# Optimization experiments

Hardware: AMD Instinct MI355X
Metric: run time of the kernel (lower is better)

## Reference

```python
import jax, jax.numpy as jnp
import numpy as np

B, N, FIN, FOUT = 8, 2048, 128, 128


def setup_inputs() -> dict:
    key = jax.random.key(0)
    k1, k2, k3, k4, k5 = jax.random.split(key, 5)
    x = jax.random.normal(k1, (B, N, FIN), dtype=jnp.float32)
    adj = jax.random.randint(k2, (N, N), 0, 2, dtype=jnp.int32)
    # W stored [in, out] (transpose of torch Linear weight; same math via x @ W)
    W = jax.random.normal(k3, (FIN, FOUT), dtype=jnp.float32) * (1.0 / np.sqrt(FIN))
    # a: Linear(2*out, 1) split into src/dst halves: a([h_i,h_j]) = h_i@a_src + h_j@a_dst
    a_src = jax.random.normal(k4, (FOUT,), dtype=jnp.float32) * 0.1
    a_dst = jax.random.normal(k5, (FOUT,), dtype=jnp.float32) * 0.1
    return {"x": x, "adj": adj, "W": W, "a_src": a_src, "a_dst": a_dst}


def reference(x, adj, W, a_src, a_dst):
    # h: [B, N, FOUT]
    h = jnp.einsum('bnf,fo->bno', x, W)
    # attention logits e_ij = LeakyReLU(a_src.h_i + a_dst.h_j), built by broadcast
    s_i = jnp.einsum('bno,o->bn', h, a_src)  # [B, N]
    s_j = jnp.einsum('bno,o->bn', h, a_dst)  # [B, N]
    e = jax.nn.leaky_relu(s_i[:, :, None] + s_j[:, None, :], negative_slope=0.2)  # [B,N,N]
    scores = jnp.where(adj[None, :, :] == 0, -jnp.inf, e)
    attn = jax.nn.softmax(scores, axis=-1)
    attn = jnp.nan_to_num(attn, nan=0.0)  # rows with no neighbors -> all zeros
    # dropout is identity in eval mode
    out = jnp.einsum('bij,bjo->bio', attn, h)  # [B, N, FOUT]
    return out
```

## Files before the change

kernel.cpp:

```cpp
#include <hip/hip_runtime.h>
#include <math.h>

#define BATCH 8
#define NN 2048
#define FF 128

typedef __attribute__((ext_vector_type(4))) float f32x4;
typedef _Float16 half8 __attribute__((ext_vector_type(8)));

__device__ __forceinline__ unsigned short h2u(_Float16 h) {
    return __builtin_bit_cast(unsigned short, h);
}

__device__ __forceinline__ void h_split(float f, unsigned short& hi, unsigned short& lo) {
    const _Float16 hh = (_Float16)f;
    hi = h2u(hh);
    lo = h2u((_Float16)(f - (float)hh));
}

__global__ __launch_bounds__(256) void k_prep(const int* __restrict__ adj,
                                              const float* __restrict__ W,
                                              unsigned short* __restrict__ Wf_hi,
                                              unsigned short* __restrict__ Wf_lo,
                                              unsigned* __restrict__ amT) {
    const int t = threadIdx.x;
    const int bx = blockIdx.x;
    if (bx < 512) {
        const int w = t >> 6, lane = t & 63;
        const int row = bx * 4 + w;
        const int* __restrict__ ar = adj + (size_t)row * NN;
        #pragma unroll 8
        for (int seg = 0; seg < 32; ++seg) {
            const unsigned long long m = __ballot(ar[seg * 64 + lane] != 0);
            if (lane == 0)  amT[(size_t)(seg * 2) * NN + row] = (unsigned)m;
            if (lane == 32) amT[(size_t)(seg * 2 + 1) * NN + row] = (unsigned)(m >> 32);
        }
    } else {
        #pragma unroll
        for (int e = 0; e < 8; ++e) {
            const int fi = (bx - 512) * 2048 + e * 256 + t;
            const int j = fi & 7, ln = (fi >> 3) & 63, nt = (fi >> 9) & 7, ks = fi >> 12;
            const int k = ks * 32 + (ln >> 4) * 8 + j;
            const int col = nt * 16 + (ln & 15);
            unsigned short hh, hl;
            h_split(W[k * FF + col], hh, hl);
            Wf_hi[fi] = hh;
            Wf_lo[fi] = hl;
        }
    }
}

__global__ __launch_bounds__(256) void k_h(const float* __restrict__ x,
                                           const unsigned short* __restrict__ Wf_hi,
                                           const unsigned short* __restrict__ Wf_lo,
                                           const float* __restrict__ a_src,
                                           const float* __restrict__ a_dst,
                                           unsigned short* __restrict__ hF,
                                           float* __restrict__ Eg,  float* __restrict__ E2g,
                                           float* __restrict__ Sg,  float* __restrict__ S2g) {
    __shared__ float sred[4 * 16];
    __shared__ float dred[4 * 16];

    const int t = threadIdx.x;
    const int w = t >> 6, lane = t & 63;
    const int nl = lane & 15, quad = lane >> 4;
    const int row0 = blockIdx.x * 16;
    const int b = row0 >> 11, jloc0 = row0 & 2047;
    const int gr = row0 + nl;
    const int nt0 = w * 2;

    f32x4 acc[2] = {{0.f,0.f,0.f,0.f},{0.f,0.f,0.f,0.f}};

    #pragma unroll
    for (int ks = 0; ks < 4; ++ks) {
        const float4 xa = *reinterpret_cast<const float4*>(&x[(size_t)gr * FF + ks * 32 + quad * 8]);
        const float4 xb = *reinterpret_cast<const float4*>(&x[(size_t)gr * FF + ks * 32 + quad * 8 + 4]);
        const float xv[8] = {xa.x, xa.y, xa.z, xa.w, xb.x, xb.y, xb.z, xb.w};
        half8 ah, al;
        #pragma unroll
        for (int i = 0; i < 8; ++i) {
            const _Float16 hh = (_Float16)xv[i];
            ah[i] = hh;
            al[i] = (_Float16)(xv[i] - (float)hh);
        }
        #pragma unroll
        for (int nn = 0; nn < 2; ++nn) {
            const int bo = ((ks * 8 + nt0 + nn) * 64 + lane) * 8;
            const half8 bh = *reinterpret_cast<const half8*>(&Wf_hi[bo]);
            const half8 bl = *reinterpret_cast<const half8*>(&Wf_lo[bo]);
            acc[nn] = __builtin_amdgcn_mfma_f32_16x16x32_f16(ah, bh, acc[nn], 0, 0, 0);
            acc[nn] = __builtin_amdgcn_mfma_f32_16x16x32_f16(al, bh, acc[nn], 0, 0, 0);
            acc[nn] = __builtin_amdgcn_mfma_f32_16x16x32_f16(ah, bl, acc[nn], 0, 0, 0);
        }
    }

    const int jloc = jloc0 + quad * 4;
    const int jg = jloc >> 3, u0 = jloc & 7;
    #pragma unroll
    for (int nn = 0; nn < 2; ++nn) {
        ushort4 hv;
        hv.x = h2u((_Float16)acc[nn][0]);
        hv.y = h2u((_Float16)acc[nn][1]);
        hv.z = h2u((_Float16)acc[nn][2]);
        hv.w = h2u((_Float16)acc[nn][3]);
        *reinterpret_cast<ushort4*>(&hF[(size_t)b * 262144 + (nt0 + nn) * 32768 + jg * 128 + nl * 8 + u0]) = hv;
    }

    float as[2], ad[2];
    #pragma unroll
    for (int nn = 0; nn < 2; ++nn) {
        const int col = (nt0 + nn) * 16 + nl;
        as[nn] = a_src[col];
        ad[nn] = a_dst[col];
    }
    #pragma unroll
    for (int r = 0; r < 4; ++r) {
        float sp = acc[0][r] * as[0] + acc[1][r] * as[1];
        float dp = acc[0][r] * ad[0] + acc[1][r] * ad[1];
        #pragma unroll
        for (int off = 8; off >= 1; off >>= 1) {
            sp += __shfl_xor(sp, off, 16);
            dp += __shfl_xor(dp, off, 16);
        }
        if (nl == 0) {
            sred[w * 16 + quad * 4 + r] = sp;
            dred[w * 16 + quad * 4 + r] = dp;
        }
    }
    __syncthreads();
    if (t < 16) {
        const float sp = sred[t] + sred[16 + t] + sred[32 + t] + sred[48 + t];
        const float dp = dred[t] + dred[16 + t] + dred[32 + t] + dred[48 + t];
        const int row = row0 + t;
        Sg[row]  = __expf(sp - 2.f);
        S2g[row] = __expf(0.2f * sp - 2.f);
        Eg[row]  = __expf(dp - 2.f);
        E2g[row] = __expf(0.2f * dp - 2.f);
    }
}

__global__ __launch_bounds__(512, 4) void k_attn(const unsigned short* __restrict__ hF,
                                                 const unsigned* __restrict__ amT,
                                                 const float* __restrict__ Eg,
                                                 const float* __restrict__ E2g,
                                                 const float* __restrict__ Sg,
                                                 const float* __restrict__ S2g,
                                                 float* __restrict__ P,
                                                 float* __restrict__ L) {
    __shared__ float E_l[1024];
    __shared__ float E2_l[1024];
    __shared__ unsigned am_l[32 * 64];
    __shared__ unsigned short pA[2 * 64 * 72];

    const int t = threadIdx.x;
    const int b = blockIdx.y;
    const int i0 = blockIdx.x * 64;
    const int jh = blockIdx.z;
    const int jbase = jh * 1024;

    *reinterpret_cast<float2*>(&E_l[t * 2])  = *reinterpret_cast<const float2*>(&Eg[(size_t)b * NN + jbase + t * 2]);
    *reinterpret_cast<float2*>(&E2_l[t * 2]) = *reinterpret_cast<const float2*>(&E2g[(size_t)b * NN + jbase + t * 2]);
    #pragma unroll
    for (int k = 0; k < 4; ++k) {
        const int idx = k * 512 + t;
        am_l[idx] = amT[(size_t)(jh * 32 + (idx >> 6)) * NN + i0 + (idx & 63)];
    }
    __syncthreads();

    const int rp = t >> 4, jw4 = t & 15;
    const int ra = rp * 2, rb = ra + 1;
    const float Sa  = Sg[(size_t)b * NN + i0 + ra];
    const float S2a = S2g[(size_t)b * NN + i0 + ra];
    const float Sb  = Sg[(size_t)b * NN + i0 + rb];
    const float S2b = S2g[(size_t)b * NN + i0 + rb];
    const int bitb = (jw4 & 7) * 4;
    const int pwo = ra * 72 + jw4 * 4;

    const int w = t >> 6, lane = t & 63;
    const int nl = lane & 15, quad = lane >> 4;
    const int mtp = w & 1, ntp = w >> 1;
    const unsigned short* __restrict__ hFb = hF + (size_t)b * 262144;
    int bofs[2], aofs[2];
    #pragma unroll
    for (int nn = 0; nn < 2; ++nn) bofs[nn] = (ntp + nn * 4) * 32768 + (jbase + quad * 8) * 16 + nl * 8;
    #pragma unroll
    for (int mm = 0; mm < 2; ++mm) aofs[mm] = ((mtp + mm * 2) * 16 + nl) * 72 + quad * 8;

    f32x4 acc[2][2] = {{{0.f,0.f,0.f,0.f},{0.f,0.f,0.f,0.f}},{{0.f,0.f,0.f,0.f},{0.f,0.f,0.f,0.f}}};
    f32x4 lac[2] = {{0.f,0.f,0.f,0.f},{0.f,0.f,0.f,0.f}};
    half8 ones;
    #pragma unroll
    for (int i = 0; i < 8; ++i) ones[i] = (_Float16)1.f;

    for (int tt = 0; tt < 16; ++tt) {
        const int buf = tt & 1;
        const int jofs = tt * 1024;

        half8 bfr[2][2];
        #pragma unroll
        for (int nn = 0; nn < 2; ++nn) {
            bfr[nn][0] = *reinterpret_cast<const half8*>(hFb + bofs[nn] + jofs);
            bfr[nn][1] = *reinterpret_cast<const half8*>(hFb + bofs[nn] + jofs + 512);
        }

        {
            const int jb = tt * 64 + jw4 * 4;
            const float4 ej4  = *reinterpret_cast<const float4*>(&E_l[jb]);
            const float4 e2j4 = *reinterpret_cast<const float4*>(&E2_l[jb]);
            const uint2 mw = *reinterpret_cast<const uint2*>(&am_l[(tt * 2 + (jw4 >> 3)) * 64 + ra]);
            const float ejA[4]  = {ej4.x, ej4.y, ej4.z, ej4.w};
            const float e2jA[4] = {e2j4.x, e2j4.y, e2j4.z, e2j4.w};
            ushort4 ha, hb;
            #pragma unroll
            for (int jj = 0; jj < 4; ++jj) {
                const float ua = fmaxf(Sa * ejA[jj], S2a * e2jA[jj]);
                const float ub = fmaxf(Sb * ejA[jj], S2b * e2jA[jj]);
                const float pa = ((mw.x >> (bitb + jj)) & 1u) ? ua : 0.f;
                const float pb = ((mw.y >> (bitb + jj)) & 1u) ? ub : 0.f;
                ((unsigned short*)&ha)[jj] = h2u((_Float16)pa);
                ((unsigned short*)&hb)[jj] = h2u((_Float16)pb);
            }
            *reinterpret_cast<ushort4*>(&pA[buf * 4608 + pwo]) = ha;
            *reinterpret_cast<ushort4*>(&pA[buf * 4608 + pwo + 72]) = hb;
        }

        __syncthreads();

        half8 afr[2][2];
        #pragma unroll
        for (int mm = 0; mm < 2; ++mm) {
            afr[mm][0] = *reinterpret_cast<const half8*>(&pA[buf * 4608 + aofs[mm]]);
            afr[mm][1] = *reinterpret_cast<const half8*>(&pA[buf * 4608 + aofs[mm] + 32]);
        }
        #pragma unroll
        for (int mm = 0; mm < 2; ++mm) {
            #pragma unroll
            for (int kh = 0; kh < 2; ++kh) {
                lac[mm] = __builtin_amdgcn_mfma_f32_16x16x32_f16(afr[mm][kh], ones, lac[mm], 0, 0, 0);
                acc[mm][0] = __builtin_amdgcn_mfma_f32_16x16x32_f16(afr[mm][kh], bfr[0][kh], acc[mm][0], 0, 0, 0);
                acc[mm][1] = __builtin_amdgcn_mfma_f32_16x16x32_f16(afr[mm][kh], bfr[1][kh], acc[mm][1], 0, 0, 0);
            }
        }
    }

    float* __restrict__ Pb = P + ((size_t)jh * BATCH + b) * 262144;
    float* __restrict__ Lb = L + ((size_t)jh * BATCH + b) * 2048;
    #pragma unroll
    for (int mm = 0; mm < 2; ++mm) {
        const int lrow = (mtp + mm * 2) * 16 + quad * 4;
        #pragma unroll
        for (int r = 0; r < 4; ++r) {
            #pragma unroll
            for (int nn = 0; nn < 2; ++nn) {
                const int col = (ntp + nn * 4) * 16 + nl;
                Pb[(size_t)(i0 + lrow + r) * FF + col] = acc[mm][nn][r];
            }
            if (nl == 0 && ntp == 0) Lb[i0 + lrow + r] = lac[mm][r];
        }
    }
}

__global__ __launch_bounds__(256) void k_comb(const float* __restrict__ P,
                                              const float* __restrict__ L,
                                              float* __restrict__ out) {
    const int g0 = blockIdx.x * 512 + threadIdx.x;
    #pragma unroll
    for (int it = 0; it < 2; ++it) {
        const int g = g0 + it * 256;
        const size_t flat = (size_t)g * 4;
        const int row = (int)(flat >> 7);
        const float l = L[row] + L[16384 + row];
        const float inv = (l > 0.f) ? 1.f / l : 0.f;
        const float4 p0 = *reinterpret_cast<const float4*>(&P[flat]);
        const float4 p1 = *reinterpret_cast<const float4*>(&P[2097152 + flat]);
        *reinterpret_cast<float4*>(&out[flat]) =
            make_float4((p0.x + p1.x) * inv, (p0.y + p1.y) * inv,
                        (p0.z + p1.z) * inv, (p0.w + p1.w) * inv);
    }
}

extern "C" void kernel_launch(void* const* d_in, const int* in_sizes, int n_in,
                              void* d_out, int out_size, void* d_ws, size_t ws_size,
                              hipStream_t stream) {
    const float* x     = (const float*)d_in[0];
    const int*   adj   = (const int*)d_in[1];
    const float* W     = (const float*)d_in[2];
    const float* a_src = (const float*)d_in[3];
    const float* a_dst = (const float*)d_in[4];
    float* out = (float*)d_out;

    unsigned short* hF    = (unsigned short*)d_ws;
    unsigned short* Wf_hi = hF + 2097152;
    unsigned short* Wf_lo = Wf_hi + 16384;
    float* Eg  = (float*)(Wf_lo + 16384);
    float* E2g = Eg + 16384;
    float* Sg  = E2g + 16384;
    float* S2g = Sg + 16384;
    unsigned* amT = (unsigned*)(S2g + 16384);
    float* P = (float*)(amT + 131072);
    float* L = P + 4194304;

    k_prep<<<520, 256, 0, stream>>>(adj, W, Wf_hi, Wf_lo, amT);
    k_h<<<1024, 256, 0, stream>>>(x, Wf_hi, Wf_lo, a_src, a_dst, hF, Eg, E2g, Sg, S2g);
    k_attn<<<dim3(32, BATCH, 2), 512, 0, stream>>>(hF, amT, Eg, E2g, Sg, S2g, P, L);
    k_comb<<<1024, 256, 0, stream>>>(P, L, out);
}
```

Before: 117.6 us.

## Fuse prep into projection kernel, split attention 4-way, combine via last-block counter

Removes the separate prep kernel by packing adjacency bitmasks and converting W to split fp16 inside the projection kernel, and removes the combine kernel by having the last of four j-split attention blocks reduce partials using an atomic counter. The attention grid grows from 2 to 4 j-splits, which doubles the block count for occupancy but doubles partial P traffic. W is now read and split per block from global memory instead of being precomputed once, adding redundant loads and conversions.

```diff
diff --git a/kernel.cpp b/kernel.cpp
--- a/kernel.cpp
+++ b/kernel.cpp
@@ -12,52 +12,16 @@
     return __builtin_bit_cast(unsigned short, h);
 }
 
-__device__ __forceinline__ void h_split(float f, unsigned short& hi, unsigned short& lo) {
-    const _Float16 hh = (_Float16)f;
-    hi = h2u(hh);
-    lo = h2u((_Float16)(f - (float)hh));
-}
-
-__global__ __launch_bounds__(256) void k_prep(const int* __restrict__ adj,
-                                              const float* __restrict__ W,
-                                              unsigned short* __restrict__ Wf_hi,
-                                              unsigned short* __restrict__ Wf_lo,
-                                              unsigned* __restrict__ amT) {
-    const int t = threadIdx.x;
-    const int bx = blockIdx.x;
-    if (bx < 512) {
-        const int w = t >> 6, lane = t & 63;
-        const int row = bx * 4 + w;
-        const int* __restrict__ ar = adj + (size_t)row * NN;
-        #pragma unroll 8
-        for (int seg = 0; seg < 32; ++seg) {
-            const unsigned long long m = __ballot(ar[seg * 64 + lane] != 0);
-            if (lane == 0)  amT[(size_t)(seg * 2) * NN + row] = (unsigned)m;
-            if (lane == 32) amT[(size_t)(seg * 2 + 1) * NN + row] = (unsigned)(m >> 32);
-        }
-    } else {
-        #pragma unroll
-        for (int e = 0; e < 8; ++e) {
-            const int fi = (bx - 512) * 2048 + e * 256 + t;
-            const int j = fi & 7, ln = (fi >> 3) & 63, nt = (fi >> 9) & 7, ks = fi >> 12;
-            const int k = ks * 32 + (ln >> 4) * 8 + j;
-            const int col = nt * 16 + (ln & 15);
-            unsigned short hh, hl;
-            h_split(W[k * FF + col], hh, hl);
-            Wf_hi[fi] = hh;
-            Wf_lo[fi] = hl;
-        }
-    }
-}
-
 __global__ __launch_bounds__(256) void k_h(const float* __restrict__ x,
-                                           const unsigned short* __restrict__ Wf_hi,
-                                           const unsigned short* __restrict__ Wf_lo,
+                                           const int* __restrict__ adj,
+                                           const float* __restrict__ W,
                                            const float* __restrict__ a_src,
                                            const float* __restrict__ a_dst,
                                            unsigned short* __restrict__ hF,
                                            float* __restrict__ Eg,  float* __restrict__ E2g,
-                                           float* __restrict__ Sg,  float* __restrict__ S2g) {
+                                           float* __restrict__ Sg,  float* __restrict__ S2g,
+                                           unsigned* __restrict__ amT,
+                                           unsigned* __restrict__ cnt) {
     __shared__ float sred[4 * 16];
     __shared__ float dred[4 * 16];
 
@@ -69,6 +33,21 @@
     const int gr = row0 + nl;
     const int nt0 = w * 2;
 
+    if (blockIdx.x == 0) cnt[t] = 0;
+
+    {
+        const int prow = blockIdx.x * 2 + (w >> 1);
+        const int* __restrict__ ar = adj + (size_t)prow * NN;
+        const int s0 = (w & 1) * 16;
+        #pragma unroll
+        for (int s = 0; s < 16; ++s) {
+            const int seg = s0 + s;
+            const unsigned long long m = __ballot(ar[seg * 64 + lane] != 0);
+            if (lane == 0)  amT[(size_t)(seg * 2) * NN + prow] = (unsigned)m;
+            if (lane == 32) amT[(size_t)(seg * 2 + 1) * NN + prow] = (unsigned)(m >> 32);
+        }
+    }
+
     f32x4 acc[2] = {{0.f,0.f,0.f,0.f},{0.f,0.f,0.f,0.f}};
 
     #pragma unroll
@@ -85,9 +64,15 @@
         }
         #pragma unroll
         for (int nn = 0; nn < 2; ++nn) {
-            const int bo = ((ks * 8 + nt0 + nn) * 64 + lane) * 8;
-            const half8 bh = *reinterpret_cast<const half8*>(&Wf_hi[bo]);
-            const half8 bl = *reinterpret_cast<const half8*>(&Wf_lo[bo]);
+            const float* __restrict__ wp = W + (size_t)(ks * 32 + quad * 8) * FF + (nt0 + nn) * 16 + nl;
+            half8 bh, bl;
+            #pragma unroll
+            for (int j = 0; j < 8; ++j) {
+                const float wv = wp[j * FF];
+                const _Float16 hh = (_Float16)wv;
+                bh[j] = hh;
+                bl[j] = (_Float16)(wv - (float)hh);
+            }
             acc[nn] = __builtin_amdgcn_mfma_f32_16x16x32_f16(ah, bh, acc[nn], 0, 0, 0);
             acc[nn] = __builtin_amdgcn_mfma_f32_16x16x32_f16(al, bh, acc[nn], 0, 0, 0);
             acc[nn] = __builtin_amdgcn_mfma_f32_16x16x32_f16(ah, bl, acc[nn], 0, 0, 0);
@@ -146,24 +131,27 @@
                                                  const float* __restrict__ Sg,
                                                  const float* __restrict__ S2g,
                                                  float* __restrict__ P,
-                                                 float* __restrict__ L) {
-    __shared__ float E_l[1024];
-    __shared__ float E2_l[1024];
-    __shared__ unsigned am_l[32 * 64];
+                                                 float* __restrict__ L,
+                                                 unsigned* __restrict__ cnt,
+                                                 float* __restrict__ out) {
+    __shared__ float E_l[512];
+    __shared__ float E2_l[512];
+    __shared__ unsigned am_l[16 * 64];
     __shared__ unsigned short pA[2 * 64 * 72];
+    __shared__ int last_s;
 
     const int t = threadIdx.x;
     const int b = blockIdx.y;
     const int i0 = blockIdx.x * 64;
     const int jh = blockIdx.z;
-    const int jbase = jh * 1024;
-
-    *reinterpret_cast<float2*>(&E_l[t * 2])  = *reinterpret_cast<const float2*>(&Eg[(size_t)b * NN + jbase + t * 2]);
-    *reinterpret_cast<float2*>(&E2_l[t * 2]) = *reinterpret_cast<const float2*>(&E2g[(size_t)b * NN + jbase + t * 2]);
-    #pragma unroll
-    for (int k = 0; k < 4; ++k) {
+    const int jbase = jh * 512;
+
+    E_l[t]  = Eg[(size_t)b * NN + jbase + t];
+    E2_l[t] = E2g[(size_t)b * NN + jbase + t];
+    #pragma unroll
+    for (int k = 0; k < 2; ++k) {
         const int idx = k * 512 + t;
-        am_l[idx] = amT[(size_t)(jh * 32 + (idx >> 6)) * NN + i0 + (idx & 63)];
+        am_l[idx] = amT[(size_t)(jh * 16 + (idx >> 6)) * NN + i0 + (idx & 63)];
     }
     __syncthreads();
 
@@ -192,7 +180,7 @@
     #pragma unroll
     for (int i = 0; i < 8; ++i) ones[i] = (_Float16)1.f;
 
-    for (int tt = 0; tt < 16; ++tt) {
+    for (int tt = 0; tt < 8; ++tt) {
         const int buf = tt & 1;
         const int jofs = tt * 1024;
 
@@ -258,24 +246,38 @@
             if (nl == 0 && ntp == 0) Lb[i0 + lrow + r] = lac[mm][r];
         }
     }
-}
-
-__global__ __launch_bounds__(256) void k_comb(const float* __restrict__ P,
-                                              const float* __restrict__ L,
-                                              float* __restrict__ out) {
-    const int g0 = blockIdx.x * 512 + threadIdx.x;
-    #pragma unroll
-    for (int it = 0; it < 2; ++it) {
-        const int g = g0 + it * 256;
-        const size_t flat = (size_t)g * 4;
-        const int row = (int)(flat >> 7);
-        const float l = L[row] + L[16384 + row];
+
+    __threadfence();
+    __syncthreads();
+    if (t == 0) {
+        const unsigned old = atomicAdd(&cnt[b * 32 + blockIdx.x], 1u);
+        last_s = (old == 3u);
+    }
+    __syncthreads();
+    if (last_s) {
+        __threadfence();
+        const int row = t >> 3;
+        const int cg = (t & 7) * 16;
+        float l = 0.f;
+        #pragma unroll
+        for (int q = 0; q < 4; ++q) l += L[((size_t)q * BATCH + b) * 2048 + i0 + row];
         const float inv = (l > 0.f) ? 1.f / l : 0.f;
-        const float4 p0 = *reinterpret_cast<const float4*>(&P[flat]);
-        const float4 p1 = *reinterpret_cast<const float4*>(&P[2097152 + flat]);
-        *reinterpret_cast<float4*>(&out[flat]) =
-            make_float4((p0.x + p1.x) * inv, (p0.y + p1.y) * inv,
-                        (p0.z + p1.z) * inv, (p0.w + p1.w) * inv);
+        float4 s[4] = {{0,0,0,0},{0,0,0,0},{0,0,0,0},{0,0,0,0}};
+        #pragma unroll
+        for (int q = 0; q < 4; ++q) {
+            const float* __restrict__ Pp = P + ((size_t)q * BATCH + b) * 262144 + (size_t)(i0 + row) * FF + cg;
+            #pragma unroll
+            for (int v = 0; v < 4; ++v) {
+                const float4 pv = *reinterpret_cast<const float4*>(&Pp[v * 4]);
+                s[v].x += pv.x; s[v].y += pv.y; s[v].z += pv.z; s[v].w += pv.w;
+            }
+        }
+        float* __restrict__ op = out + ((size_t)b * NN + i0 + row) * FF + cg;
+        #pragma unroll
+        for (int v = 0; v < 4; ++v) {
+            *reinterpret_cast<float4*>(&op[v * 4]) =
+                make_float4(s[v].x * inv, s[v].y * inv, s[v].z * inv, s[v].w * inv);
+        }
     }
 }
 
@@ -289,19 +291,16 @@
     const float* a_dst = (const float*)d_in[4];
     float* out = (float*)d_out;
 
-    unsigned short* hF    = (unsigned short*)d_ws;
-    unsigned short* Wf_hi = hF + 2097152;
-    unsigned short* Wf_lo = Wf_hi + 16384;
-    float* Eg  = (float*)(Wf_lo + 16384);
+    unsigned short* hF = (unsigned short*)d_ws;
+    float* Eg  = (float*)(hF + 2097152);
     float* E2g = Eg + 16384;
     float* Sg  = E2g + 16384;
     float* S2g = Sg + 16384;
     unsigned* amT = (unsigned*)(S2g + 16384);
     float* P = (float*)(amT + 131072);
-    float* L = P + 4194304;
-
-    k_prep<<<520, 256, 0, stream>>>(adj, W, Wf_hi, Wf_lo, amT);
-    k_h<<<1024, 256, 0, stream>>>(x, Wf_hi, Wf_lo, a_src, a_dst, hF, Eg, E2g, Sg, S2g);
-    k_attn<<<dim3(32, BATCH, 2), 512, 0, stream>>>(hF, amT, Eg, E2g, Sg, S2g, P, L);
-    k_comb<<<1024, 256, 0, stream>>>(P, L, out);
+    float* L = P + 8388608;
+    unsigned* cnt = (unsigned*)(L + 65536);
+
+    k_h<<<1024, 256, 0, stream>>>(x, adj, W, a_src, a_dst, hF, Eg, E2g, Sg, S2g, amT, cnt);
+    k_attn<<<dim3(32, BATCH, 4), 512, 0, stream>>>(hF, amT, Eg, E2g, Sg, S2g, P, L, cnt, out);
 }
```

Measured after the change: 395.2 us. 3.36x slower.
